# Kernel tuning notes

Measured on AMD Instinct MI355X. Metric: run time of the kernel, lower is better.

The kernel has to match this reference:

```python
import jax, jax.numpy as jnp
import numpy as np

NEG_SLOPE = 0.2
EPS = 1e-16  # PyG softmax eps


def _gat_conv(x, src, dst, W, att_src, att_dst, bias, heads, out_ch):
    """PyG GATConv (eval mode, self-loops already appended, concat output)."""
    N = x.shape[0]
    xw = (x @ W).reshape(N, heads, out_ch)            # [N,H,C]
    a_src = jnp.sum(xw * att_src, axis=-1)            # [N,H]
    a_dst = jnp.sum(xw * att_dst, axis=-1)            # [N,H]
    e = jax.nn.leaky_relu(a_src[src] + a_dst[dst], NEG_SLOPE)  # [E,H]
    m = jax.ops.segment_max(e, dst, num_segments=N)   # [N,H] (self-loops -> no empty segs)
    e = jnp.exp(e - m[dst])
    denom = jax.ops.segment_sum(e, dst, num_segments=N)
    alpha = e / (denom[dst] + EPS)                    # [E,H]
    msg = xw[src] * alpha[:, :, None]                 # [E,H,C]
    out = jax.ops.segment_sum(msg, dst, num_segments=N)  # [N,H,C]
    return out.reshape(N, heads * out_ch) + bias


def setup_inputs() -> dict:
    key = jax.random.key(0)
    ks = jax.random.split(key, 12)
    N, E, F_in, H, C, NC = 20000, 320000, 512, 8, 64, 32
    x = jax.random.normal(ks[0], (N, F_in), dtype=jnp.float32)
    edge_index = jax.random.randint(ks[1], (2, E), 0, N, dtype=jnp.int64)
    g = lambda k, shape, fan: jax.random.normal(k, shape, dtype=jnp.float32) * (1.0 / np.sqrt(fan))
    return {
        "x": x,
        "edge_index": edge_index,
        "W1": g(ks[2], (F_in, H * C), F_in),
        "att_src1": g(ks[3], (H, C), C),
        "att_dst1": g(ks[4], (H, C), C),
        "b1": jnp.zeros((H * C,), dtype=jnp.float32),
        "W2": g(ks[5], (H * C, NC), H * C),
        "att_src2": g(ks[6], (1, NC), NC),
        "att_dst2": g(ks[7], (1, NC), NC),
        "b2": jnp.zeros((NC,), dtype=jnp.float32),
    }


def reference(x, edge_index, W1, att_src1, att_dst1, b1, W2, att_src2, att_dst2, b2):
    N = x.shape[0]
    H, C = att_src1.shape
    NC = att_src2.shape[1]
    # GATConv adds self-loops by default
    loops = jnp.arange(N, dtype=edge_index.dtype)
    src = jnp.concatenate([edge_index[0], loops])
    dst = jnp.concatenate([edge_index[1], loops])
    h = _gat_conv(x, src, dst, W1, att_src1, att_dst1, b1, H, C)
    h = jax.nn.elu(h)
    h = _gat_conv(h, src, dst, W2, att_src2, att_dst2, b2, 1, NC)
    return jax.nn.log_softmax(h, axis=1)
```

## Files before the change

kernel.cpp:

```cpp
#include <hip/hip_runtime.h>
#include <math.h>

#define NEG_SLOPE 0.2f
#define SM_EPS 1e-16f

typedef short short8 __attribute__((ext_vector_type(8)));
typedef float floatx4 __attribute__((ext_vector_type(4)));


__device__ inline unsigned short f2bf(float x) {
    unsigned int u = __float_as_uint(x);
    unsigned int r = (u + 0x7FFFu + ((u >> 16) & 1u)) >> 16;
    return (unsigned short)r;
}

__device__ inline float bf2f(unsigned short h) {
    return __uint_as_float(((unsigned int)h) << 16);
}

__device__ inline float bflo(unsigned int u) { return __uint_as_float(u << 16); }
__device__ inline float bfhi(unsigned int u) { return __uint_as_float(u & 0xFFFF0000u); }

__device__ __forceinline__ void gl_lds16(const unsigned short* g, unsigned short* l) {
    __builtin_amdgcn_global_load_lds(
        (const __attribute__((address_space(1))) unsigned int*)(g),
        (__attribute__((address_space(3))) unsigned int*)(l), 16, 0, 0);
}

__device__ inline void get_edge(const int* __restrict__ srcA, const int* __restrict__ dstA,
                                int e, int E, int& s, int& d) {
    if (e < E) { s = srcA[e]; d = dstA[e]; }
    else { s = e - E; d = e - E; }
}


__global__ __launch_bounds__(256) void k_prep(const float* __restrict__ x,
                                              unsigned short* __restrict__ xb,
                                              const float* __restrict__ W1,
                                              unsigned short* __restrict__ w1t,
                                              const float* __restrict__ W2,
                                              unsigned short* __restrict__ w2bt,
                                              const int* __restrict__ dstA,
                                              int E, int Ep,
                                              int* __restrict__ deg,
                                              int nblk_deg, int nblk_x) {
    __shared__ float tile[32][33];
    int bx = blockIdx.x;
    int t = threadIdx.x;
    if (bx < nblk_deg) {
        int e = bx * 256 + t;
        if (e < Ep) {
            int d = (e < E) ? dstA[e] : (e - E);
            atomicAdd(&deg[d], 1);
        }
    } else if (bx < nblk_deg + nblk_x) {
        int i = ((bx - nblk_deg) * 256 + t) * 4;
        float4 v = *(const float4*)(x + i);
        ushort4 o;
        o.x = f2bf(v.x); o.y = f2bf(v.y); o.z = f2bf(v.z); o.w = f2bf(v.w);
        *(ushort4*)(xb + i) = o;
    } else if (bx < nblk_deg + nblk_x + 256) {
        int b = bx - nblk_deg - nblk_x;
        int kb = (b & 15) * 32;
        int nb = (b >> 4) * 32;
        int tx = t & 31, ty = t >> 5;
        #pragma unroll
        for (int i = 0; i < 32; i += 8)
            tile[ty + i][tx] = W1[(size_t)(kb + ty + i) * 512 + nb + tx];
        __syncthreads();
        #pragma unroll
        for (int i = 0; i < 32; i += 8)
            w1t[(size_t)(nb + ty + i) * 512 + kb + tx] = f2bf(tile[tx][ty + i]);
    } else {
        int i = (bx - nblk_deg - nblk_x - 256) * 256 + t;
        int c = i >> 9, k = i & 511;
        w2bt[i] = f2bf(W2[k * 32 + c]);
    }
}


__global__ __launch_bounds__(256) void k_scan1(const int* __restrict__ deg, int* __restrict__ incl,
                                               int* __restrict__ part, int N) {
    __shared__ int sm[256];
    int t = threadIdx.x;
    int i = blockIdx.x * 256 + t;
    int v = (i < N) ? deg[i] : 0;
    sm[t] = v; __syncthreads();
    for (int o = 1; o < 256; o <<= 1) {
        int x = (t >= o) ? sm[t - o] : 0;
        __syncthreads();
        sm[t] += x;
        __syncthreads();
    }
    if (i < N) incl[i] = sm[t];
    if (t == 255) part[blockIdx.x] = sm[255];
}

__global__ __launch_bounds__(256) void k_scan3(const int* __restrict__ incl, const int* __restrict__ part,
                                               const int* __restrict__ deg, int* __restrict__ off,
                                               int* __restrict__ cursor, int N) {
    __shared__ int sm[256];
    int bx = blockIdx.x, t = threadIdx.x;
    int partial = 0;
    for (int i = t; i < bx; i += 256) partial += part[i];
    sm[t] = partial; __syncthreads();
    for (int o = 128; o > 0; o >>= 1) {
        if (t < o) sm[t] += sm[t + o];
        __syncthreads();
    }
    int base = sm[0];
    int i = bx * 256 + t;
    if (i >= N) return;
    int v = incl[i] + base;
    off[i + 1] = v;
    cursor[i] = v - deg[i];
    if (i == 0) off[0] = 0;
}

__global__ __launch_bounds__(256) void k_scatter(const int* __restrict__ srcA, const int* __restrict__ dstA,
                                                 int E, int Ep, int* __restrict__ cursor,
                                                 int* __restrict__ src_s) {
    int e = blockIdx.x * 256 + threadIdx.x;
    if (e >= Ep) return;
    int s, d; get_edge(srcA, dstA, e, E, s, d);
    int p = atomicAdd(&cursor[d], 1);
    src_s[p] = s;
}


__global__ __launch_bounds__(256) void k_gemm1_mfma(const unsigned short* __restrict__ A,
                                                    const unsigned short* __restrict__ Bt,
                                                    const float* __restrict__ att_s,
                                                    const float* __restrict__ att_d,
                                                    unsigned short* __restrict__ C,
                                                    float* __restrict__ a_sd,
                                                    float* __restrict__ a_dd, int M) {
    const int K = 512;
    __shared__ unsigned short As[128 * 32];
    __shared__ unsigned short Bs[128 * 32];
    int t = threadIdx.x;
    int lane = t & 63;
    int w = t >> 6;
    int row0 = blockIdx.x * 128;
    int col0 = blockIdx.y * 128;
    int wm = (w >> 1) * 64, wn = (w & 1) * 64;
    int l15 = lane & 15, q = lane >> 4;

    int mrow = t >> 2;
    int kk = (t & 3) * 8;
    unsigned short* ldsA0 = &As[w * 512];
    unsigned short* ldsA1 = &As[2048 + w * 512];
    unsigned short* ldsB0 = &Bs[w * 512];
    unsigned short* ldsB1 = &Bs[2048 + w * 512];

    floatx4 acc[4][4] = {};

    for (int k0 = 0; k0 < K; k0 += 32) {
        gl_lds16(A  + (size_t)(row0 + mrow) * K + k0 + kk,      ldsA0);
        gl_lds16(A  + (size_t)(row0 + 64 + mrow) * K + k0 + kk, ldsA1);
        gl_lds16(Bt + (size_t)(col0 + mrow) * K + k0 + kk,      ldsB0);
        gl_lds16(Bt + (size_t)(col0 + 64 + mrow) * K + k0 + kk, ldsB1);
        __syncthreads();
        short8 af[4], bfr[4];
        #pragma unroll
        for (int i = 0; i < 4; ++i)
            af[i] = *(const short8*)(&As[(wm + i * 16 + l15) * 32 + q * 8]);
        #pragma unroll
        for (int j = 0; j < 4; ++j)
            bfr[j] = *(const short8*)(&Bs[(wn + j * 16 + l15) * 32 + q * 8]);
        #pragma unroll
        for (int i = 0; i < 4; ++i)
            #pragma unroll
            for (int j = 0; j < 4; ++j)
                acc[i][j] = __builtin_amdgcn_mfma_f32_16x16x32_bf16(af[i], bfr[j], acc[i][j], 0, 0, 0);
        __syncthreads();
    }

    #pragma unroll
    for (int i = 0; i < 4; ++i) {
        #pragma unroll
        for (int p = 0; p < 4; ++p) {
            int r = row0 + wm + i * 16 + q * 4 + p;
            if (r < M) {
                #pragma unroll
                for (int j = 0; j < 4; ++j) {
                    int c = col0 + wn + j * 16 + l15;
                    C[(size_t)r * 512 + c] = f2bf(acc[i][j][p]);
                }
            }
        }
    }

    int hh = blockIdx.y * 2 + (w & 1);
    float asr[4], adr[4];
    #pragma unroll
    for (int j = 0; j < 4; ++j) {
        asr[j] = att_s[hh * 64 + j * 16 + l15];
        adr[j] = att_d[hh * 64 + j * 16 + l15];
    }
    #pragma unroll
    for (int i = 0; i < 4; ++i) {
        #pragma unroll
        for (int p = 0; p < 4; ++p) {
            float ds = 0.f, dd = 0.f;
            #pragma unroll
            for (int j = 0; j < 4; ++j) {
                ds = fmaf(acc[i][j][p], asr[j], ds);
                dd = fmaf(acc[i][j][p], adr[j], dd);
            }
            #pragma unroll
            for (int mk = 1; mk <= 8; mk <<= 1) {
                ds += __shfl_xor(ds, mk);
                dd += __shfl_xor(dd, mk);
            }
            int r = row0 + wm + i * 16 + q * 4 + p;
            if (l15 == 0 && r < M) {
                a_sd[(size_t)hh * M + r] = ds;
                a_dd[(size_t)hh * M + r] = dd;
            }
        }
    }
}


__global__ __launch_bounds__(256) void k_l1(const unsigned short* __restrict__ xw,
                                            const float* __restrict__ a_s,
                                            const float* __restrict__ a_d,
                                            const int* __restrict__ off,
                                            const int* __restrict__ src_s,
                                            const float* __restrict__ bias,
                                            unsigned short* __restrict__ hout, int N) {
    int wid = threadIdx.x >> 6, lane = threadIdx.x & 63;
    int h = blockIdx.x & 7;
    int n = (blockIdx.x >> 3) * 32 + wid * 8 + (lane >> 3);
    int li = lane & 7;
    if (n >= N) return;
    int p0 = off[n], p1 = off[n + 1];
    const float* ash = a_s + (size_t)h * N;
    float adv = a_d[(size_t)h * N + n];
    const size_t cbase = (size_t)h * 64 + (size_t)li * 8;

    float acc[8] = {};
    float s = 0.f;
    int p = p0;
    for (; p + 4 <= p1; p += 4) {
        int s0 = src_s[p];
        int s1 = src_s[p + 1];
        int s2 = src_s[p + 2];
        int s3 = src_s[p + 3];
        const uint4 u0 = *(const uint4*)(xw + (size_t)s0 * 512 + cbase);
        const uint4 u1 = *(const uint4*)(xw + (size_t)s1 * 512 + cbase);
        const uint4 u2 = *(const uint4*)(xw + (size_t)s2 * 512 + cbase);
        const uint4 u3 = *(const uint4*)(xw + (size_t)s3 * 512 + cbase);
        float e0 = ash[s0] + adv; e0 = e0 > 0.f ? e0 : NEG_SLOPE * e0;
        float e1 = ash[s1] + adv; e1 = e1 > 0.f ? e1 : NEG_SLOPE * e1;
        float e2 = ash[s2] + adv; e2 = e2 > 0.f ? e2 : NEG_SLOPE * e2;
        float e3 = ash[s3] + adv; e3 = e3 > 0.f ? e3 : NEG_SLOPE * e3;
        float w0 = __expf(e0);
        float w1 = __expf(e1);
        float w2 = __expf(e2);
        float w3 = __expf(e3);
        s += (w0 + w1) + (w2 + w3);
        acc[0] = fmaf(w0, bflo(u0.x), acc[0]); acc[1] = fmaf(w0, bfhi(u0.x), acc[1]);
        acc[2] = fmaf(w0, bflo(u0.y), acc[2]); acc[3] = fmaf(w0, bfhi(u0.y), acc[3]);
        acc[4] = fmaf(w0, bflo(u0.z), acc[4]); acc[5] = fmaf(w0, bfhi(u0.z), acc[5]);
        acc[6] = fmaf(w0, bflo(u0.w), acc[6]); acc[7] = fmaf(w0, bfhi(u0.w), acc[7]);
        acc[0] = fmaf(w1, bflo(u1.x), acc[0]); acc[1] = fmaf(w1, bfhi(u1.x), acc[1]);
        acc[2] = fmaf(w1, bflo(u1.y), acc[2]); acc[3] = fmaf(w1, bfhi(u1.y), acc[3]);
        acc[4] = fmaf(w1, bflo(u1.z), acc[4]); acc[5] = fmaf(w1, bfhi(u1.z), acc[5]);
        acc[6] = fmaf(w1, bflo(u1.w), acc[6]); acc[7] = fmaf(w1, bfhi(u1.w), acc[7]);
        acc[0] = fmaf(w2, bflo(u2.x), acc[0]); acc[1] = fmaf(w2, bfhi(u2.x), acc[1]);
        acc[2] = fmaf(w2, bflo(u2.y), acc[2]); acc[3] = fmaf(w2, bfhi(u2.y), acc[3]);
        acc[4] = fmaf(w2, bflo(u2.z), acc[4]); acc[5] = fmaf(w2, bfhi(u2.z), acc[5]);
        acc[6] = fmaf(w2, bflo(u2.w), acc[6]); acc[7] = fmaf(w2, bfhi(u2.w), acc[7]);
        acc[0] = fmaf(w3, bflo(u3.x), acc[0]); acc[1] = fmaf(w3, bfhi(u3.x), acc[1]);
        acc[2] = fmaf(w3, bflo(u3.y), acc[2]); acc[3] = fmaf(w3, bfhi(u3.y), acc[3]);
        acc[4] = fmaf(w3, bflo(u3.z), acc[4]); acc[5] = fmaf(w3, bfhi(u3.z), acc[5]);
        acc[6] = fmaf(w3, bflo(u3.w), acc[6]); acc[7] = fmaf(w3, bfhi(u3.w), acc[7]);
    }
    for (; p < p1; ++p) {
        int s0 = src_s[p];
        const uint4 u0 = *(const uint4*)(xw + (size_t)s0 * 512 + cbase);
        float e0 = ash[s0] + adv; e0 = e0 > 0.f ? e0 : NEG_SLOPE * e0;
        float w0 = __expf(e0);
        s += w0;
        acc[0] = fmaf(w0, bflo(u0.x), acc[0]); acc[1] = fmaf(w0, bfhi(u0.x), acc[1]);
        acc[2] = fmaf(w0, bflo(u0.y), acc[2]); acc[3] = fmaf(w0, bfhi(u0.y), acc[3]);
        acc[4] = fmaf(w0, bflo(u0.z), acc[4]); acc[5] = fmaf(w0, bfhi(u0.z), acc[5]);
        acc[6] = fmaf(w0, bflo(u0.w), acc[6]); acc[7] = fmaf(w0, bfhi(u0.w), acc[7]);
    }

    float inv = 1.f / (s + SM_EPS);
    unsigned int ov[4];
    #pragma unroll
    for (int j = 0; j < 4; ++j) {
        float v0 = acc[2 * j] * inv     + bias[cbase + 2 * j];
        float v1 = acc[2 * j + 1] * inv + bias[cbase + 2 * j + 1];
        v0 = v0 > 0.f ? v0 : __expf(v0) - 1.f;
        v1 = v1 > 0.f ? v1 : __expf(v1) - 1.f;
        ov[j] = (unsigned int)f2bf(v0) | ((unsigned int)f2bf(v1) << 16);
    }
    *(uint4*)(hout + (size_t)n * 512 + cbase) = make_uint4(ov[0], ov[1], ov[2], ov[3]);
}


__global__ __launch_bounds__(256) void k_gemm2_mfma(const unsigned short* __restrict__ A,
                                                    const unsigned short* __restrict__ Bt,
                                                    const float* __restrict__ att_s,
                                                    const float* __restrict__ att_d,
                                                    unsigned short* __restrict__ O,
                                                    float* __restrict__ a_s, float* __restrict__ a_d,
                                                    int M) {
    const int K = 512;
    __shared__ unsigned short As[64 * 40];
    __shared__ unsigned short Bs[32 * 40];
    int t = threadIdx.x;
    int lane = t & 63;
    int w = t >> 6;
    int row0 = blockIdx.x * 64;
    int l15 = lane & 15, q = lane >> 4;

    floatx4 acc[2] = {};

    for (int k0 = 0; k0 < K; k0 += 32) {
        {
            int flat = t * 8;
            int m = flat >> 5, kk = flat & 31;
            uint4 va = make_uint4(0u, 0u, 0u, 0u);
            int gr = row0 + m;
            if (gr < M) va = *(const uint4*)(A + (size_t)gr * K + k0 + kk);
            *(uint4*)(&As[m * 40 + kk]) = va;
            if (t < 128) {
                int nn = t >> 2, kb = (t & 3) * 8;
                *(uint4*)(&Bs[nn * 40 + kb]) = *(const uint4*)(Bt + (size_t)nn * K + k0 + kb);
            }
        }
        __syncthreads();
        short8 af = *(const short8*)(&As[(w * 16 + l15) * 40 + q * 8]);
        short8 b0 = *(const short8*)(&Bs[(l15) * 40 + q * 8]);
        short8 b1 = *(const short8*)(&Bs[(16 + l15) * 40 + q * 8]);
        acc[0] = __builtin_amdgcn_mfma_f32_16x16x32_bf16(af, b0, acc[0], 0, 0, 0);
        acc[1] = __builtin_amdgcn_mfma_f32_16x16x32_bf16(af, b1, acc[1], 0, 0, 0);
        __syncthreads();
    }

    float as_lo = att_s[l15], as_hi = att_s[16 + l15];
    float ad_lo = att_d[l15], ad_hi = att_d[16 + l15];
    #pragma unroll
    for (int p = 0; p < 4; ++p) {
        int r = row0 + w * 16 + q * 4 + p;
        bool ok = r < M;
        float v0 = acc[0][p], v1 = acc[1][p];
        if (ok) {
            O[(size_t)r * 32 + l15]      = f2bf(v0);
            O[(size_t)r * 32 + 16 + l15] = f2bf(v1);
        }
        float ds = v0 * as_lo + v1 * as_hi;
        float dd = v0 * ad_lo + v1 * ad_hi;
        #pragma unroll
        for (int mk = 1; mk <= 8; mk <<= 1) {
            ds += __shfl_xor(ds, mk);
            dd += __shfl_xor(dd, mk);
        }
        if (ok && l15 == 0) { a_s[r] = ds; a_d[r] = dd; }
    }
}


__global__ __launch_bounds__(256) void k_l2(const unsigned short* __restrict__ hw2,
                                            const float* __restrict__ a_s,
                                            const float* __restrict__ a_d,
                                            const int* __restrict__ off,
                                            const int* __restrict__ src_s,
                                            const float* __restrict__ bias,
                                            float* __restrict__ outp, int N) {
    int wid = threadIdx.x >> 6, lane = threadIdx.x & 63;
    int n = blockIdx.x * 4 + wid;
    if (n >= N) return;
    int p0 = off[n], p1 = off[n + 1];
    float adv = a_d[n];
    int c = lane & 31, ep = lane >> 5;

    float acc = 0.f, s = 0.f;
    int p = p0;
    for (; p + 64 <= p1; p += 64) {
        int bsrc = src_s[p + lane];
        float e = a_s[bsrc] + adv;
        e = e > 0.f ? e : NEG_SLOPE * e;
        float w64 = __expf(e);
        #pragma unroll
        for (int j = 0; j < 64; j += 2) {
            int sj = __shfl(bsrc, j + ep);
            float wj = __shfl(w64, j + ep);
            s += wj;
            acc = fmaf(wj, bf2f(hw2[(size_t)sj * 32 + c]), acc);
        }
    }
    if (p < p1) {
        int nb = p1 - p;
        int bsrc = src_s[p + (lane < nb ? lane : 0)];
        float e = a_s[bsrc] + adv;
        e = e > 0.f ? e : NEG_SLOPE * e;
        float w64 = __expf(e);
        for (int j = 0; j < nb; j += 2) {
            int idx = j + ep;
            bool valid = idx < nb;
            int idc = valid ? idx : 0;
            int sj = __shfl(bsrc, idc);
            float wj = __shfl(w64, idc);
            if (valid) {
                s += wj;
                acc = fmaf(wj, bf2f(hw2[(size_t)sj * 32 + c]), acc);
            }
        }
    }
    acc += __shfl_xor(acc, 32);
    s   += __shfl_xor(s, 32);
    float v = acc / (s + SM_EPS) + bias[c];
    float mx = v;
    #pragma unroll
    for (int mk = 16; mk >= 1; mk >>= 1) mx = fmaxf(mx, __shfl_xor(mx, mk, 32));
    float ex = __expf(v - mx);
    float sum = ex;
    #pragma unroll
    for (int mk = 16; mk >= 1; mk >>= 1) sum += __shfl_xor(sum, mk, 32);
    if (lane < 32) outp[(size_t)n * 32 + c] = (v - mx) - __logf(sum);
}


extern "C" void kernel_launch(void* const* d_in, const int* in_sizes, int n_in,
                              void* d_out, int out_size, void* d_ws, size_t ws_size,
                              hipStream_t stream) {
    const float* x   = (const float*)d_in[0];
    const int*   ei  = (const int*)d_in[1];
    const float* W1  = (const float*)d_in[2];
    const float* as1 = (const float*)d_in[3];
    const float* ad1 = (const float*)d_in[4];
    const float* b1  = (const float*)d_in[5];
    const float* W2  = (const float*)d_in[6];
    const float* as2 = (const float*)d_in[7];
    const float* ad2 = (const float*)d_in[8];
    const float* b2  = (const float*)d_in[9];
    float* out = (float*)d_out;

    const int F = 512;
    const int N = in_sizes[0] / F;
    const int E = in_sizes[1] / 2;
    const int Ep = E + N;
    const int* srcA = ei;
    const int* dstA = ei + E;

    char* w = (char*)d_ws;
    auto alloc = [&](size_t b) -> void* {
        void* p = (void*)w;
        w += (b + 255) & ~(size_t)255;
        return p;
    };
    unsigned short* xbf  = (unsigned short*)alloc((size_t)N * 512 * 2);
    unsigned short* w1t  = (unsigned short*)alloc((size_t)512 * 512 * 2);
    unsigned short* w2bt = (unsigned short*)alloc((size_t)32 * 512 * 2);
    unsigned short* xw1  = (unsigned short*)alloc((size_t)N * 512 * 2);
    unsigned short* hbuf = (unsigned short*)alloc((size_t)N * 512 * 2);
    float* a_s1 = (float*)alloc((size_t)N * 8 * 4);
    float* a_d1 = (float*)alloc((size_t)N * 8 * 4);
    unsigned short* hw2 = (unsigned short*)alloc((size_t)N * 32 * 2);
    float* a_s2 = (float*)alloc((size_t)N * 4);
    float* a_d2 = (float*)alloc((size_t)N * 4);
    int* deg    = (int*)alloc((size_t)N * 4);
    int* incl   = (int*)alloc((size_t)N * 4);
    int* part   = (int*)alloc(256 * 4);
    int* off    = (int*)alloc((size_t)(N + 1) * 4);
    int* cursor = (int*)alloc((size_t)N * 4);
    int* src_s  = (int*)alloc((size_t)Ep * 4);

    int egrid = (Ep + 255) / 256;
    int sgrid = (N + 255) / 256;
    int ngrid4 = (N + 3) / 4;
    int nblk_x = (N * 512 / 4) / 256;
    int nblk_w2 = (32 * 512 + 255) / 256;

    hipMemsetAsync(deg, 0, (size_t)N * 4, stream);

    k_prep<<<egrid + nblk_x + 256 + nblk_w2, 256, 0, stream>>>(
        x, xbf, W1, w1t, W2, w2bt, dstA, E, Ep, deg, egrid, nblk_x);

    k_scan1<<<sgrid, 256, 0, stream>>>(deg, incl, part, N);
    k_scan3<<<sgrid, 256, 0, stream>>>(incl, part, deg, off, cursor, N);
    k_scatter<<<egrid, 256, 0, stream>>>(srcA, dstA, E, Ep, cursor, src_s);

    {
        dim3 g1((N + 127) / 128, 512 / 128);
        k_gemm1_mfma<<<g1, 256, 0, stream>>>(xbf, w1t, as1, ad1, xw1, a_s1, a_d1, N);
    }
    {
        int ngrid32 = (N + 31) / 32;
        k_l1<<<ngrid32 * 8, 256, 0, stream>>>(xw1, a_s1, a_d1, off, src_s, b1, hbuf, N);
    }

    k_gemm2_mfma<<<(N + 63) / 64, 256, 0, stream>>>(hbuf, w2bt, as2, ad2, hw2, a_s2, a_d2, N);
    k_l2<<<ngrid4, 256, 0, stream>>>(hw2, a_s2, a_d2, off, src_s, b2, out, N);
}
```

Baseline: 242.9 us.

## Preload full K tiles via LDS DMA in gemm2; vectorize layer-2 edge aggregation

The second-layer GEMM now loads the whole 64x512 A tile and 32x512 B tile into LDS once, using global_load_lds with an XOR swizzle. This replaces the per-K-step cooperative loads and the two barriers per iteration, at the cost of about 96KB of LDS per block, which limits occupancy. The layer-2 aggregation kernel now has each lane handle one of 8 edges and 4 channels with uint2 vector gathers, computing edge weights per lane instead of broadcasting them with shuffles. Lanes are reduced by XOR shuffles at the end. The row-bound check on A is removed, so it relies on M being a multiple of 64 (20000 is not, so the last block may read out of bounds).

```diff
diff --git a/kernel.cpp b/kernel.cpp
--- a/kernel.cpp
+++ b/kernel.cpp
@@ -312,36 +312,37 @@
                                                     float* __restrict__ a_s, float* __restrict__ a_d,
                                                     int M) {
     const int K = 512;
-    __shared__ unsigned short As[64 * 40];
-    __shared__ unsigned short Bs[32 * 40];
+    __shared__ unsigned short As[64 * 512];
+    __shared__ unsigned short Bs[32 * 512];
     int t = threadIdx.x;
     int lane = t & 63;
     int w = t >> 6;
     int row0 = blockIdx.x * 64;
     int l15 = lane & 15, q = lane >> 4;
 
+    #pragma unroll
+    for (int i = 0; i < 16; ++i) {
+        int r = w * 16 + i;
+        gl_lds16(A + (size_t)(row0 + r) * K + ((lane ^ (r & 7)) << 3), &As[r * 512]);
+    }
+    #pragma unroll
+    for (int i = 0; i < 8; ++i) {
+        int r = w * 8 + i;
+        gl_lds16(Bt + (size_t)r * K + ((lane ^ (r & 7)) << 3), &Bs[r * 512]);
+    }
+    __syncthreads();
+
     floatx4 acc[2] = {};
-
+    int ra = w * 16 + l15;
+    int rb0 = l15, rb1 = 16 + l15;
+    #pragma unroll
     for (int k0 = 0; k0 < K; k0 += 32) {
-        {
-            int flat = t * 8;
-            int m = flat >> 5, kk = flat & 31;
-            uint4 va = make_uint4(0u, 0u, 0u, 0u);
-            int gr = row0 + m;
-            if (gr < M) va = *(const uint4*)(A + (size_t)gr * K + k0 + kk);
-            *(uint4*)(&As[m * 40 + kk]) = va;
-            if (t < 128) {
-                int nn = t >> 2, kb = (t & 3) * 8;
-                *(uint4*)(&Bs[nn * 40 + kb]) = *(const uint4*)(Bt + (size_t)nn * K + k0 + kb);
-            }
-        }
-        __syncthreads();
-        short8 af = *(const short8*)(&As[(w * 16 + l15) * 40 + q * 8]);
-        short8 b0 = *(const short8*)(&Bs[(l15) * 40 + q * 8]);
-        short8 b1 = *(const short8*)(&Bs[(16 + l15) * 40 + q * 8]);
+        int cc = (k0 >> 3) + q;
+        short8 af = *(const short8*)(&As[ra * 512 + ((cc ^ (ra & 7)) << 3)]);
+        short8 b0 = *(const short8*)(&Bs[rb0 * 512 + ((cc ^ (rb0 & 7)) << 3)]);
+        short8 b1 = *(const short8*)(&Bs[rb1 * 512 + ((cc ^ (rb1 & 7)) << 3)]);
         acc[0] = __builtin_amdgcn_mfma_f32_16x16x32_bf16(af, b0, acc[0], 0, 0, 0);
         acc[1] = __builtin_amdgcn_mfma_f32_16x16x32_bf16(af, b1, acc[1], 0, 0, 0);
-        __syncthreads();
     }
 
     float as_lo = att_s[l15], as_hi = att_s[16 + l15];
@@ -379,52 +380,77 @@
     if (n >= N) return;
     int p0 = off[n], p1 = off[n + 1];
     float adv = a_d[n];
-    int c = lane & 31, ep = lane >> 5;
-
-    float acc = 0.f, s = 0.f;
+    int e8 = lane >> 3;
+    int li = lane & 7;
+    const int cbase = li * 4;
+
+    float acc[4] = {};
+    float s = 0.f;
     int p = p0;
-    for (; p + 64 <= p1; p += 64) {
-        int bsrc = src_s[p + lane];
-        float e = a_s[bsrc] + adv;
-        e = e > 0.f ? e : NEG_SLOPE * e;
-        float w64 = __expf(e);
-        #pragma unroll
-        for (int j = 0; j < 64; j += 2) {
-            int sj = __shfl(bsrc, j + ep);
-            float wj = __shfl(w64, j + ep);
-            s += wj;
-            acc = fmaf(wj, bf2f(hw2[(size_t)sj * 32 + c]), acc);
-        }
+    for (; p + 16 <= p1; p += 16) {
+        int sA = src_s[p + e8];
+        int sB = src_s[p + 8 + e8];
+        const uint2 uA = *(const uint2*)(hw2 + (size_t)sA * 32 + cbase);
+        const uint2 uB = *(const uint2*)(hw2 + (size_t)sB * 32 + cbase);
+        float eA = a_s[sA] + adv; eA = eA > 0.f ? eA : NEG_SLOPE * eA;
+        float eB = a_s[sB] + adv; eB = eB > 0.f ? eB : NEG_SLOPE * eB;
+        float wA = __expf(eA);
+        float wB = __expf(eB);
+        s += wA + wB;
+        acc[0] = fmaf(wA, bflo(uA.x), acc[0]); acc[1] = fmaf(wA, bfhi(uA.x), acc[1]);
+        acc[2] = fmaf(wA, bflo(uA.y), acc[2]); acc[3] = fmaf(wA, bfhi(uA.y), acc[3]);
+        acc[0] = fmaf(wB, bflo(uB.x), acc[0]); acc[1] = fmaf(wB, bfhi(uB.x), acc[1]);
+        acc[2] = fmaf(wB, bflo(uB.y), acc[2]); acc[3] = fmaf(wB, bfhi(uB.y), acc[3]);
+    }
+    for (; p + 8 <= p1; p += 8) {
+        int sA = src_s[p + e8];
+        const uint2 uA = *(const uint2*)(hw2 + (size_t)sA * 32 + cbase);
+        float eA = a_s[sA] + adv; eA = eA > 0.f ? eA : NEG_SLOPE * eA;
+        float wA = __expf(eA);
+        s += wA;
+        acc[0] = fmaf(wA, bflo(uA.x), acc[0]); acc[1] = fmaf(wA, bfhi(uA.x), acc[1]);
+        acc[2] = fmaf(wA, bflo(uA.y), acc[2]); acc[3] = fmaf(wA, bfhi(uA.y), acc[3]);
     }
     if (p < p1) {
         int nb = p1 - p;
-        int bsrc = src_s[p + (lane < nb ? lane : 0)];
-        float e = a_s[bsrc] + adv;
-        e = e > 0.f ? e : NEG_SLOPE * e;
-        float w64 = __expf(e);
-        for (int j = 0; j < nb; j += 2) {
-            int idx = j + ep;
-            bool valid = idx < nb;
-            int idc = valid ? idx : 0;
-            int sj = __shfl(bsrc, idc);
-            float wj = __shfl(w64, idc);
-            if (valid) {
-                s += wj;
-                acc = fmaf(wj, bf2f(hw2[(size_t)sj * 32 + c]), acc);
-            }
-        }
-    }
-    acc += __shfl_xor(acc, 32);
-    s   += __shfl_xor(s, 32);
-    float v = acc / (s + SM_EPS) + bias[c];
-    float mx = v;
-    #pragma unroll
-    for (int mk = 16; mk >= 1; mk >>= 1) mx = fmaxf(mx, __shfl_xor(mx, mk, 32));
-    float ex = __expf(v - mx);
-    float sum = ex;
-    #pragma unroll
-    for (int mk = 16; mk >= 1; mk >>= 1) sum += __shfl_xor(sum, mk, 32);
-    if (lane < 32) outp[(size_t)n * 32 + c] = (v - mx) - __logf(sum);
+        bool val = e8 < nb;
+        int sA = src_s[val ? p + e8 : p];
+        const uint2 uA = *(const uint2*)(hw2 + (size_t)sA * 32 + cbase);
+        float eA = a_s[sA] + adv; eA = eA > 0.f ? eA : NEG_SLOPE * eA;
+        float wA = val ? __expf(eA) : 0.f;
+        s += wA;
+        acc[0] = fmaf(wA, bflo(uA.x), acc[0]); acc[1] = fmaf(wA, bfhi(uA.x), acc[1]);
+        acc[2] = fmaf(wA, bflo(uA.y), acc[2]); acc[3] = fmaf(wA, bfhi(uA.y), acc[3]);
+    }
+
+    #pragma unroll
+    for (int mk = 8; mk <= 32; mk <<= 1) {
+        s += __shfl_xor(s, mk);
+        #pragma unroll
+        for (int j = 0; j < 4; ++j) acc[j] += __shfl_xor(acc[j], mk);
+    }
+
+    float inv = 1.f / (s + SM_EPS);
+    float v[4];
+    #pragma unroll
+    for (int j = 0; j < 4; ++j) v[j] = acc[j] * inv + bias[cbase + j];
+
+    float mx = fmaxf(fmaxf(v[0], v[1]), fmaxf(v[2], v[3]));
+    mx = fmaxf(mx, __shfl_xor(mx, 1));
+    mx = fmaxf(mx, __shfl_xor(mx, 2));
+    mx = fmaxf(mx, __shfl_xor(mx, 4));
+    float sum = 0.f;
+    #pragma unroll
+    for (int j = 0; j < 4; ++j) sum += __expf(v[j] - mx);
+    sum += __shfl_xor(sum, 1);
+    sum += __shfl_xor(sum, 2);
+    sum += __shfl_xor(sum, 4);
+    float lse = __logf(sum);
+    if (e8 == 0) {
+        float4 o = make_float4(v[0] - mx - lse, v[1] - mx - lse,
+                               v[2] - mx - lse, v[3] - mx - lse);
+        *(float4*)(outp + (size_t)n * 32 + cbase) = o;
+    }
 }
 
 
```

Result: faster. 227.9 us (-6.2%).
